# Performance work log

Hardware: AMD Instinct MI355X
Metric: run time of the kernel (lower is better)

The kernel has to match this reference:

```python
import jax, jax.numpy as jnp
import numpy as np
from jax import lax


def setup_inputs() -> dict:
    key = jax.random.key(0)
    k1, k2, k3 = jax.random.split(key, 3)
    B, Ci, Co, K, H, W = 8, 512, 512, 3, 32, 32
    x = jax.random.normal(k1, (B, Ci, H, W), dtype=jnp.float32)
    y_s = jax.random.normal(k2, (B, Ci), dtype=jnp.float32)
    weight = jax.random.normal(k3, (Co, Ci, K, K), dtype=jnp.float32)  # scale_init = 1 (equal_lr)
    bias = jnp.zeros((Co,), dtype=jnp.float32)
    return {"x": x, "y_s": y_s, "weight": weight, "bias": bias}


def reference(x, y_s, weight, bias):
    # equal_lr=True -> runtime scale = (in_channels * k^2) ** -0.5
    Co, Ci, K, _ = weight.shape
    scale_forward = (Ci * K * K) ** -0.5
    w = scale_forward * weight  # [Co, Ci, K, K]

    # Fused StyleGAN2 trick (mathematically identical to per-sample grouped conv):
    # conv(x, y_s[b,i]*w[o,i]) == conv(x * y_s, w); demod divides by per-(b,o) norm.
    x_mod = x * y_s[:, :, None, None]
    out = lax.conv_general_dilated(
        x_mod, w,
        window_strides=(1, 1),
        padding=((1, 1), (1, 1)),
        rhs_dilation=(1, 1),
        dimension_numbers=("NCHW", "OIHW", "NCHW"),
    )  # [B, Co, H, W]

    # demod=True: x_s[b,o] = sqrt(sum_{i,kh,kw} (y_s[b,i]*w[o,i,kh,kw])^2 + 1e-8)
    w2 = jnp.sum(w * w, axis=(2, 3))  # [Co, Ci]
    xs = jnp.sqrt(jnp.einsum("bi,oi->bo", y_s * y_s, w2) + 1e-8)  # [B, Co]
    out = out / xs[:, :, None, None] + bias[None, :, None, None]
    return out
```

## Files before the change

### kernel.cpp

```cpp
#include <hip/hip_runtime.h>

typedef __attribute__((ext_vector_type(8))) short short8;
typedef __attribute__((ext_vector_type(4))) float f32x4;

#define RCP_OFF   0
#define WPRE_OFF  16384
#define XM_OFF    4734976

__device__ __forceinline__ unsigned short f2bf(float f) {
  unsigned int u = __float_as_uint(f);
  u += 0x7FFFu + ((u >> 16) & 1u);
  return (unsigned short)(u >> 16);
}

__device__ __forceinline__ void gload_lds16(const void* g, void* l) {
  __builtin_amdgcn_global_load_lds(
      (__attribute__((address_space(1))) void*)g,
      (__attribute__((address_space(3))) void*)l, 16, 0, 0);
}

__global__ __launch_bounds__(256) void prep_kernel(
    const float* __restrict__ x, const float* __restrict__ ys,
    const float* __restrict__ w,
    unsigned short* __restrict__ xm, unsigned short* __restrict__ wpre,
    float* __restrict__ rcp) {
  int bid = blockIdx.x;
  int tid = threadIdx.x;

  if (bid < 512) {
    int half = bid & 1;
    int h = (bid >> 1) & 31;
    int b = bid >> 6;
    __shared__ float tile[256][33];
    int ci0 = half * 256;
#pragma unroll
    for (int r = 0; r < 32; ++r) {
      int ci = r * 8 + (tid >> 5);
      int wcol = tid & 31;
      float v = x[(((size_t)b * 512 + ci0 + ci) * 32 + h) * 32 + wcol];
      tile[ci][wcol] = v * ys[b * 512 + ci0 + ci];
    }
    __syncthreads();
    int g0 = half * 32;
    for (int r = 0; r < 5; ++r) {
      int idx = r * 256 + tid;
      if (idx < 1088) {
        int gl = idx / 34;
        int col = idx - gl * 34;
        short8 v = {0,0,0,0,0,0,0,0};
        if (col != 0 && col != 33) {
          int wcol = col - 1;
#pragma unroll
          for (int j = 0; j < 8; ++j)
            v[j] = (short)f2bf(tile[gl * 8 + j][wcol]);
        }
        size_t off = ((((size_t)b * 64 + g0 + gl) * 34 + (h + 1)) * 34 + col) * 8;
        *reinterpret_cast<short8*>(xm + off) = v;
      }
    }
    if (h == 0 || h == 31) {
      int hp = (h == 0) ? 0 : 33;
      for (int r = 0; r < 5; ++r) {
        int idx = r * 256 + tid;
        if (idx < 1088) {
          int gl = idx / 34;
          int col = idx - gl * 34;
          short8 z = {0,0,0,0,0,0,0,0};
          size_t off = ((((size_t)b * 64 + g0 + gl) * 34 + hp) * 34 + col) * 8;
          *reinterpret_cast<short8*>(xm + off) = z;
        }
      }
    }
  } else if (bid < 640) {
    int pid = bid - 512;
    int coh = pid & 1;
    int kb = (pid >> 1) & 7;
    int c = pid >> 4;
    int co = coh * 256 + tid;
    int ci0 = c * 64 + kb * 8;
    const float* wp = w + (size_t)co * 4608 + (size_t)ci0 * 9;
    float v[72];
    const f32x4* wp4 = reinterpret_cast<const f32x4*>(wp);
#pragma unroll
    for (int i = 0; i < 18; ++i) {
      f32x4 q = wp4[i];
      v[i * 4 + 0] = q[0]; v[i * 4 + 1] = q[1]; v[i * 4 + 2] = q[2]; v[i * 4 + 3] = q[3];
    }
    const float scale = 1.4731391274719738e-02f;
#pragma unroll
    for (int t = 0; t < 9; ++t) {
      short8 s;
#pragma unroll
      for (int j = 0; j < 8; ++j) s[j] = (short)f2bf(scale * v[j * 9 + t]);
      *reinterpret_cast<short8*>(wpre + ((((size_t)c * 9 + t) * 8 + kb) * 512 + co) * 8) = s;
    }
  } else {
    int pid = bid - 640;
    int wv = tid >> 6;
    int lane = tid & 63;
    int o = pid * 4 + wv;
    const float* wp = w + (size_t)o * 4608 + (size_t)lane * 72;
    const float scale2 = 1.0f / 4608.0f;
    float w2[8];
#pragma unroll
    for (int j = 0; j < 8; ++j) {
      float s = 0.f;
#pragma unroll
      for (int k = 0; k < 9; ++k) { float vv = wp[j * 9 + k]; s += vv * vv; }
      w2[j] = s * scale2;
    }
#pragma unroll
    for (int b = 0; b < 8; ++b) {
      float p = 0.f;
#pragma unroll
      for (int j = 0; j < 8; ++j) {
        float y = ys[b * 512 + lane * 8 + j];
        p += y * y * w2[j];
      }
#pragma unroll
      for (int off = 32; off > 0; off >>= 1) p += __shfl_down(p, off);
      if (lane == 0) rcp[b * 512 + o] = 1.0f / sqrtf(p + 1e-8f);
    }
  }
}

__global__ __launch_bounds__(512, 1) void conv_main(
    const unsigned short* __restrict__ wpre,
    const unsigned short* __restrict__ xm,
    const float* __restrict__ rcp,
    const float* __restrict__ bias,
    float* __restrict__ out)
{
  __shared__ __align__(16) char smem[52224];

  int bid = blockIdx.x;
  int xcd = bid & 7;
  int j0 = bid >> 3;
  int cog = xcd >> 1;
  int sp = (xcd & 1) * 32 + j0;
  int b = sp >> 3;
  int hg = sp & 7;
  int tid = threadIdx.x;
  int lane = tid & 63;
  int wv = tid >> 6;
  int wc = wv & 1;
  int wr = (wv >> 1) & 1;
  int kp = wv >> 2;
  int l15 = lane & 15, l4 = lane >> 4;

  f32x4 acc[4][4];
#pragma unroll
  for (int i = 0; i < 4; ++i)
#pragma unroll
    for (int jj = 0; jj < 4; ++jj) { f32x4 z = {0.f,0.f,0.f,0.f}; acc[i][jj] = z; }

  const unsigned short* xmb = xm + (size_t)b * (64 * 34 * 34 * 8);
  const unsigned short* wbase =
      wpre + ((size_t)(kp * 4 + l4) * 512 + cog * 128 + wr * 64 + l15) * 8;
  const int bbase = (kp * 4 + l4) * 3264 + wc * 2 * 544 + l15 * 16;

  auto stageX = [&](int c, int buf) {
    char* xb = smem + buf * 26112;
#pragma unroll
    for (int r = 0; r < 4; ++r) {
      int idx = r * 512 + tid;
      if (idx < 1632) {
        int kb = idx / 204;
        int rem = idx - kb * 204;
        int rr = rem / 34;
        int col = rem - rr * 34;
        const unsigned short* src =
            xmb + (((size_t)(c * 8 + kb) * 34 + hg * 4 + rr) * 34 + col) * 8;
        gload_lds16(src, xb + idx * 16);
      }
    }
  };

  auto loadA = [&](int ct, short8 (&a)[4]) {
    const unsigned short* p = wbase + (size_t)ct * 32768;
#pragma unroll
    for (int mi = 0; mi < 4; ++mi)
      a[mi] = *reinterpret_cast<const short8*>(p + mi * 128);
  };

  auto loadB = [&](const char* xb, int t, short8 (&f)[4]) {
    int kh = t / 3, kw = t % 3;
#pragma unroll
    for (int nj = 0; nj < 4; ++nj) {
      int imm = ((nj >> 1) + kh) * 544 + (nj & 1) * 256 + kw * 16;
      f[nj] = *reinterpret_cast<const short8*>(xb + bbase + imm);
    }
  };

  short8 X[4], Y[4], Z[4];

  stageX(0, 0);
  loadA(0, X);
  loadA(1, Y);
  asm volatile("s_waitcnt vmcnt(8)" ::: "memory");
  __builtin_amdgcn_s_barrier();
  asm volatile("" ::: "memory");

  for (int c = 0; c < 8; ++c) {
    const char* xb = smem + (c & 1) * 26112;
    if (c < 7) stageX(c + 1, (c + 1) & 1);
    short8 Bp[4], Bq[4];
    loadB(xb, 0, Bp);
#pragma unroll
    for (int t = 0; t < 9; ++t) {
      int ct = c * 9 + t;
      short8 (&curA)[4] = (t % 3 == 0) ? X : ((t % 3 == 1) ? Y : Z);
      short8 (&nxtA)[4] = (t % 3 == 0) ? Z : ((t % 3 == 1) ? X : Y);
      short8 (&curB)[4] = (t & 1) ? Bq : Bp;
      short8 (&nxtB)[4] = (t & 1) ? Bp : Bq;
      if (ct < 70) loadA(ct + 2, nxtA);
      __builtin_amdgcn_s_barrier();
      asm volatile("s_waitcnt lgkmcnt(0)" ::: "memory");
      __builtin_amdgcn_sched_barrier(0);
      if (t < 8) loadB(xb, t + 1, nxtB);
      __builtin_amdgcn_s_setprio(1);
#pragma unroll
      for (int nj = 0; nj < 4; ++nj)
#pragma unroll
        for (int mi = 0; mi < 4; ++mi)
          acc[mi][nj] = __builtin_amdgcn_mfma_f32_16x16x32_bf16(curA[mi], curB[nj], acc[mi][nj], 0, 0, 0);
      __builtin_amdgcn_s_setprio(0);
    }
    if (c < 7) {
      asm volatile("s_waitcnt vmcnt(8) lgkmcnt(0)" ::: "memory");
      __builtin_amdgcn_s_barrier();
      asm volatile("" ::: "memory");
    }
  }
  __syncthreads();

#pragma unroll
  for (int p = 0; p < 2; ++p) {
    if (kp == 1 && wr == p) {
#pragma unroll
      for (int mi = 0; mi < 4; ++mi)
#pragma unroll
        for (int nj = 0; nj < 4; ++nj)
          *reinterpret_cast<f32x4*>(smem + wc * 16384 + (mi * 4 + nj) * 1024 + lane * 16) = acc[mi][nj];
    }
    __syncthreads();
    if (kp == 0 && wr == p) {
#pragma unroll
      for (int mi = 0; mi < 4; ++mi)
#pragma unroll
        for (int nj = 0; nj < 4; ++nj) {
          f32x4 v = *reinterpret_cast<const f32x4*>(smem + wc * 16384 + (mi * 4 + nj) * 1024 + lane * 16);
          acc[mi][nj] = acc[mi][nj] + v;
        }
    }
    __syncthreads();
  }

  if (kp == 0) {
    const float* rcpb = rcp + b * 512;
#pragma unroll
    for (int mi = 0; mi < 4; ++mi) {
      int ob = cog * 128 + wr * 64 + mi * 16 + l4 * 4;
      float rc[4], bi[4];
#pragma unroll
      for (int jj = 0; jj < 4; ++jj) { rc[jj] = rcpb[ob + jj]; bi[jj] = bias[ob + jj]; }
#pragma unroll
      for (int nj = 0; nj < 4; ++nj) {
        int row4 = wc * 2 + (nj >> 1);
        int wcol = (nj & 1) * 16 + l15;
        int h = hg * 4 + row4;
#pragma unroll
        for (int jj = 0; jj < 4; ++jj)
          out[(((size_t)b * 512 + ob + jj) * 32 + h) * 32 + wcol] = acc[mi][nj][jj] * rc[jj] + bi[jj];
      }
    }
  }
}

extern "C" void kernel_launch(void* const* d_in, const int* in_sizes, int n_in,
                              void* d_out, int out_size, void* d_ws, size_t ws_size,
                              hipStream_t stream) {
  const float* x    = (const float*)d_in[0];
  const float* ys   = (const float*)d_in[1];
  const float* w    = (const float*)d_in[2];
  const float* bias = (const float*)d_in[3];
  float* out = (float*)d_out;
  char* ws = (char*)d_ws;
  float* rcp = (float*)(ws + RCP_OFF);
  unsigned short* wpre = (unsigned short*)(ws + WPRE_OFF);
  unsigned short* xm   = (unsigned short*)(ws + XM_OFF);

  prep_kernel<<<768, 256, 0, stream>>>(x, ys, w, xm, wpre, rcp);
  conv_main<<<256, 512, 0, stream>>>(wpre, xm, rcp, bias, out);
}
```

Before: 54.94 us.

## Fuse input modulation and bf16 packing into conv kernel staging

Drops the prep-kernel pass that wrote a padded, modulated bf16 copy of x to workspace. The conv kernel now loads fp32 x and the style vector straight into registers, multiplies them, converts to bf16 and writes the tile to LDS, with padding handled by clamped addresses and zero masks. This removes a full write and re-read of the intermediate tensor and shrinks the prep launch. In exchange it adds register pressure, more scalar global loads with 4KB strides, and redundant fp32 reads of x across output-channel groups and halo rows.

New measurement: 59.33 us. +8.0%, slower.

```diff
diff --git a/kernel.cpp b/kernel.cpp
--- a/kernel.cpp
+++ b/kernel.cpp
@@ -5,7 +5,6 @@
 
 #define RCP_OFF   0
 #define WPRE_OFF  16384
-#define XM_OFF    4734976
 
 __device__ __forceinline__ unsigned short f2bf(float f) {
   unsigned int u = __float_as_uint(f);
@@ -13,66 +12,14 @@
   return (unsigned short)(u >> 16);
 }
 
-__device__ __forceinline__ void gload_lds16(const void* g, void* l) {
-  __builtin_amdgcn_global_load_lds(
-      (__attribute__((address_space(1))) void*)g,
-      (__attribute__((address_space(3))) void*)l, 16, 0, 0);
-}
-
 __global__ __launch_bounds__(256) void prep_kernel(
-    const float* __restrict__ x, const float* __restrict__ ys,
-    const float* __restrict__ w,
-    unsigned short* __restrict__ xm, unsigned short* __restrict__ wpre,
-    float* __restrict__ rcp) {
+    const float* __restrict__ ys, const float* __restrict__ w,
+    unsigned short* __restrict__ wpre, float* __restrict__ rcp) {
   int bid = blockIdx.x;
   int tid = threadIdx.x;
 
-  if (bid < 512) {
-    int half = bid & 1;
-    int h = (bid >> 1) & 31;
-    int b = bid >> 6;
-    __shared__ float tile[256][33];
-    int ci0 = half * 256;
-#pragma unroll
-    for (int r = 0; r < 32; ++r) {
-      int ci = r * 8 + (tid >> 5);
-      int wcol = tid & 31;
-      float v = x[(((size_t)b * 512 + ci0 + ci) * 32 + h) * 32 + wcol];
-      tile[ci][wcol] = v * ys[b * 512 + ci0 + ci];
-    }
-    __syncthreads();
-    int g0 = half * 32;
-    for (int r = 0; r < 5; ++r) {
-      int idx = r * 256 + tid;
-      if (idx < 1088) {
-        int gl = idx / 34;
-        int col = idx - gl * 34;
-        short8 v = {0,0,0,0,0,0,0,0};
-        if (col != 0 && col != 33) {
-          int wcol = col - 1;
-#pragma unroll
-          for (int j = 0; j < 8; ++j)
-            v[j] = (short)f2bf(tile[gl * 8 + j][wcol]);
-        }
-        size_t off = ((((size_t)b * 64 + g0 + gl) * 34 + (h + 1)) * 34 + col) * 8;
-        *reinterpret_cast<short8*>(xm + off) = v;
-      }
-    }
-    if (h == 0 || h == 31) {
-      int hp = (h == 0) ? 0 : 33;
-      for (int r = 0; r < 5; ++r) {
-        int idx = r * 256 + tid;
-        if (idx < 1088) {
-          int gl = idx / 34;
-          int col = idx - gl * 34;
-          short8 z = {0,0,0,0,0,0,0,0};
-          size_t off = ((((size_t)b * 64 + g0 + gl) * 34 + hp) * 34 + col) * 8;
-          *reinterpret_cast<short8*>(xm + off) = z;
-        }
-      }
-    }
-  } else if (bid < 640) {
-    int pid = bid - 512;
+  if (bid < 128) {
+    int pid = bid;
     int coh = pid & 1;
     int kb = (pid >> 1) & 7;
     int c = pid >> 4;
@@ -95,7 +42,7 @@
       *reinterpret_cast<short8*>(wpre + ((((size_t)c * 9 + t) * 8 + kb) * 512 + co) * 8) = s;
     }
   } else {
-    int pid = bid - 640;
+    int pid = bid - 128;
     int wv = tid >> 6;
     int lane = tid & 63;
     int o = pid * 4 + wv;
@@ -126,7 +73,8 @@
 
 __global__ __launch_bounds__(512, 1) void conv_main(
     const unsigned short* __restrict__ wpre,
-    const unsigned short* __restrict__ xm,
+    const float* __restrict__ x,
+    const float* __restrict__ ys,
     const float* __restrict__ rcp,
     const float* __restrict__ bias,
     float* __restrict__ out)
@@ -154,24 +102,61 @@
 #pragma unroll
     for (int jj = 0; jj < 4; ++jj) { f32x4 z = {0.f,0.f,0.f,0.f}; acc[i][jj] = z; }
 
-  const unsigned short* xmb = xm + (size_t)b * (64 * 34 * 34 * 8);
   const unsigned short* wbase =
       wpre + ((size_t)(kp * 4 + l4) * 512 + cog * 128 + wr * 64 + l15) * 8;
   const int bbase = (kp * 4 + l4) * 3264 + wc * 2 * 544 + l15 * 16;
 
-  auto stageX = [&](int c, int buf) {
+  const float* xB = x + (size_t)b * 524288;
+  const float* yB = ys + b * 512;
+  int xoff_[4], ysoff_[4], ldsoff_[4];
+  bool act_[4], val_[4];
+#pragma unroll
+  for (int p = 0; p < 4; ++p) {
+    int idx = p * 512 + tid;
+    act_[p] = idx < 1632;
+    int kb = idx / 204;
+    int rem = idx - kb * 204;
+    int rr = rem / 34;
+    int col = rem - rr * 34;
+    int hr = hg * 4 - 1 + rr;
+    val_[p] = act_[p] && col >= 1 && col <= 32 && hr >= 0 && hr <= 31;
+    int hrc = min(max(hr, 0), 31);
+    int wcc = min(max(col - 1, 0), 31);
+    xoff_[p] = (kb * 8 * 32 + hrc) * 32 + wcc;
+    ysoff_[p] = kb * 8;
+    ldsoff_[p] = idx * 16;
+  }
+
+  float  xr[4][8];
+  f32x4  yr[4][2];
+
+  auto issueX = [&](int c) {
+#pragma unroll
+    for (int p = 0; p < 4; ++p) {
+      if (act_[p]) {
+        const float* xp = xB + c * 65536 + xoff_[p];
+        yr[p][0] = *reinterpret_cast<const f32x4*>(yB + c * 64 + ysoff_[p]);
+        yr[p][1] = *reinterpret_cast<const f32x4*>(yB + c * 64 + ysoff_[p] + 4);
+#pragma unroll
+        for (int j = 0; j < 8; ++j) xr[p][j] = xp[j * 1024];
+      }
+    }
+  };
+
+  auto writeX = [&](int buf) {
     char* xb = smem + buf * 26112;
 #pragma unroll
-    for (int r = 0; r < 4; ++r) {
-      int idx = r * 512 + tid;
-      if (idx < 1632) {
-        int kb = idx / 204;
-        int rem = idx - kb * 204;
-        int rr = rem / 34;
-        int col = rem - rr * 34;
-        const unsigned short* src =
-            xmb + (((size_t)(c * 8 + kb) * 34 + hg * 4 + rr) * 34 + col) * 8;
-        gload_lds16(src, xb + idx * 16);
+    for (int p = 0; p < 4; ++p) {
+      if (act_[p]) {
+        short8 v = {0,0,0,0,0,0,0,0};
+        if (val_[p]) {
+#pragma unroll
+          for (int j = 0; j < 8; ++j) {
+            float yj = (j < 4) ? yr[p][0][j] : yr[p][1][j - 4];
+            v[j] = (short)f2bf(xr[p][j] * yj);
+          }
+        }
+        *reinterpret_cast<short8*>(xb + ldsoff_[p]) = v;
       }
     }
   };
@@ -194,16 +179,18 @@
 
   short8 X[4], Y[4], Z[4];
 
-  stageX(0, 0);
+  issueX(0);
   loadA(0, X);
   loadA(1, Y);
   asm volatile("s_waitcnt vmcnt(8)" ::: "memory");
+  writeX(0);
+  asm volatile("s_waitcnt lgkmcnt(0)" ::: "memory");
   __builtin_amdgcn_s_barrier();
   asm volatile("" ::: "memory");
 
   for (int c = 0; c < 8; ++c) {
     const char* xb = smem + (c & 1) * 26112;
-    if (c < 7) stageX(c + 1, (c + 1) & 1);
+    if (c < 7) issueX(c + 1);
     short8 Bp[4], Bq[4];
     loadB(xb, 0, Bp);
 #pragma unroll
@@ -227,7 +214,9 @@
       __builtin_amdgcn_s_setprio(0);
     }
     if (c < 7) {
-      asm volatile("s_waitcnt vmcnt(8) lgkmcnt(0)" ::: "memory");
+      asm volatile("s_waitcnt vmcnt(8)" ::: "memory");
+      writeX((c + 1) & 1);
+      asm volatile("s_waitcnt lgkmcnt(0)" ::: "memory");
       __builtin_amdgcn_s_barrier();
       asm volatile("" ::: "memory");
     }
@@ -288,8 +277,7 @@
   char* ws = (char*)d_ws;
   float* rcp = (float*)(ws + RCP_OFF);
   unsigned short* wpre = (unsigned short*)(ws + WPRE_OFF);
-  unsigned short* xm   = (unsigned short*)(ws + XM_OFF);
-
-  prep_kernel<<<768, 256, 0, stream>>>(x, ys, w, xm, wpre, rcp);
-  conv_main<<<256, 512, 0, stream>>>(wpre, xm, rcp, bias, out);
-}
+
+  prep_kernel<<<256, 256, 0, stream>>>(ys, w, wpre, rcp);
+  conv_main<<<256, 512, 0, stream>>>(wpre, x, ys, rcp, bias, out);
+}
```
